# Kernel optimization log

Measured on AMD Instinct MI355X. Metric: run time of the kernel, lower is better.

Reference implementation:

```python
import jax, jax.numpy as jnp
import numpy as np
import math

HIDDEN = 1024
NUM_HEADS = 16
HEAD_DIM = 64
NUM_PREV = 4
BATCH = 4
SEQ = 1024
ROPE_BASE = 10000.0


def _rope(x):
    """Apply rotary embedding to x [..., seq, head_dim] (rotate-half form)."""
    d = x.shape[-1]
    s = x.shape[-2]
    inv_freq = 1.0 / (ROPE_BASE ** (jnp.arange(0, d, 2, dtype=jnp.float32) / d))
    ang = jnp.arange(s, dtype=jnp.float32)[:, None] * inv_freq[None, :]  # [s, d/2]
    cos, sin = jnp.cos(ang), jnp.sin(ang)
    x1, x2 = jnp.split(x, 2, axis=-1)
    return jnp.concatenate([x1 * cos - x2 * sin, x1 * sin + x2 * cos], axis=-1)


def setup_inputs() -> dict:
    key = jax.random.key(0)
    ks = jax.random.split(key, 8)
    std = 0.02
    d = {
        "hidden_states": jax.random.normal(ks[0], (BATCH, SEQ, HIDDEN), jnp.float32),
        "prev_hidden_states": jax.random.normal(ks[1], (NUM_PREV, BATCH, SEQ, HIDDEN), jnp.float32),
        "wq": jax.random.normal(ks[2], (HIDDEN, NUM_HEADS * HEAD_DIM), jnp.float32) * std,
        "bq": jnp.zeros((NUM_HEADS * HEAD_DIM,), jnp.float32),
        "wk": jax.random.normal(ks[3], (HIDDEN, NUM_HEADS * HEAD_DIM), jnp.float32) * std,
        "bk": jnp.zeros((NUM_HEADS * HEAD_DIM,), jnp.float32),
        "wv": jax.random.normal(ks[4], (HIDDEN, NUM_HEADS * HEAD_DIM), jnp.float32) * std,
        "bv": jnp.zeros((NUM_HEADS * HEAD_DIM,), jnp.float32),
        "wo": jax.random.normal(ks[5], (NUM_HEADS * HEAD_DIM, HIDDEN), jnp.float32) * std,
        "bo": jnp.zeros((HIDDEN,), jnp.float32),
        "wg": jax.random.normal(ks[6], (HIDDEN, NUM_PREV), jnp.float32) * std,
    }
    return d


def reference(hidden_states, prev_hidden_states, wq, bq, wk, bk, wv, bv, wo, bo, wg):
    B, S, H = hidden_states.shape
    P = prev_hidden_states.shape[0]
    nh, hd = NUM_HEADS, HEAD_DIM

    # Q projection + split heads + RoPE: [b, h, s, d]
    q = (hidden_states @ wq + bq).reshape(B, S, nh, hd).transpose(0, 2, 1, 3)
    q = _rope(q)

    # K/V projections for all prev layers at once: [p, b, h, s, d]
    k = (jnp.einsum('pbsh,he->pbse', prev_hidden_states, wk) + bk)
    k = k.reshape(P, B, S, nh, hd).transpose(0, 1, 3, 2, 4)
    k = _rope(k)
    v = (jnp.einsum('pbsh,he->pbse', prev_hidden_states, wv) + bv)
    v = v.reshape(P, B, S, nh, hd).transpose(0, 1, 3, 2, 4)

    # Attention per prev layer
    scale = 1.0 / math.sqrt(hd)
    attn = jnp.einsum('bhqd,pbhkd->pbhqk', q, k) * scale
    attn = jax.nn.softmax(attn, axis=-1)
    out = jnp.einsum('pbhqk,pbhkd->pbhqd', attn, v)  # [p, b, h, s, d]
    out = out.transpose(0, 1, 3, 2, 4).reshape(P, B, S, H)

    # Learned layer gating (faithful to original broadcast: requires B == P)
    pooled = jnp.mean(hidden_states, axis=1)            # [b, hidden]
    layer_w = jax.nn.softmax(pooled @ wg, axis=-1)      # [b, p]
    combined = jnp.sum(out * layer_w[:, :, None, None], axis=0)  # [b, s, hidden]

    return combined @ wo + bo
```

## Files before the change

### kernel.cpp

```cpp
#include <hip/hip_runtime.h>
#include <hip/hip_bf16.h>

#define B_  4
#define S_  1024
#define H_  1024
#define NH  16
#define HD  64
#define P_  4

typedef __attribute__((ext_vector_type(8))) short bf16x8;
typedef __attribute__((ext_vector_type(4))) float f32x4;
typedef __attribute__((ext_vector_type(16))) float f32x16;
typedef __attribute__((ext_vector_type(4))) unsigned int u32x4;

__device__ __forceinline__ float b2f(short s) {
  union { unsigned int u; float f; } v;
  v.u = ((unsigned int)(unsigned short)s) << 16;
  return v.f;
}
__device__ __forceinline__ short f2b(float f) {
  __hip_bfloat16 h = __float2bfloat16(f);
  return *reinterpret_cast<short*>(&h);
}
__device__ __forceinline__ float fast_exp2(float x) {
  float r;
  asm volatile("v_exp_f32 %0, %1" : "=v"(r) : "v"(x));
  return r;
}
__device__ __forceinline__ void gload_lds16(const void* g, void* l) {
  __builtin_amdgcn_global_load_lds(
      (const __attribute__((address_space(1))) unsigned int*)((uintptr_t)g),
      (__attribute__((address_space(3))) unsigned int*)((uintptr_t)l),
      16, 0, 0);
}

__global__ void prep_kernel(const float* __restrict__ hidden, const float* __restrict__ prev,
                            const float* __restrict__ wq, const float* __restrict__ wk,
                            const float* __restrict__ wv, const float* __restrict__ wo,
                            short* __restrict__ hbf, short* __restrict__ pbf,
                            short* __restrict__ wqT, short* __restrict__ wkT,
                            short* __restrict__ wvT, short* __restrict__ woT,
                            float* __restrict__ cost, float* __restrict__ sint,
                            float* __restrict__ pooled) {
  __shared__ short tile[32][33];
  int bid = blockIdx.x, tid = threadIdx.x;
  if (bid < 10240) {
    const float* src; short* dst; int idx;
    if (bid < 2048) { src = hidden; dst = hbf; idx = bid * 256 + tid; }
    else            { src = prev;   dst = pbf; idx = (bid - 2048) * 256 + tid; }
    const float4* s4 = (const float4*)(src + (size_t)idx * 8);
    float4 a = s4[0], b = s4[1];
    bf16x8 pk;
    pk[0] = f2b(a.x); pk[1] = f2b(a.y); pk[2] = f2b(a.z); pk[3] = f2b(a.w);
    pk[4] = f2b(b.x); pk[5] = f2b(b.y); pk[6] = f2b(b.z); pk[7] = f2b(b.w);
    *(bf16x8*)(dst + (size_t)idx * 8) = pk;
  } else if (bid < 14336) {
    int tb = bid - 10240;
    int z = tb >> 10, t = tb & 1023;
    const float* src = (z == 0) ? wq : (z == 1) ? wk : (z == 2) ? wv : wo;
    short*       dst = (z == 0) ? wqT : (z == 1) ? wkT : (z == 2) ? wvT : woT;
    int tx = tid & 31, ty = tid >> 5;
    int c0 = (t & 31) * 32, r0 = (t >> 5) * 32;
#pragma unroll
    for (int i = 0; i < 4; ++i)
      tile[ty + 8 * i][tx] = f2b(src[(r0 + ty + 8 * i) * 1024 + c0 + tx]);
    __syncthreads();
#pragma unroll
    for (int i = 0; i < 4; ++i)
      dst[(c0 + ty + 8 * i) * 1024 + r0 + tx] = tile[tx][ty + 8 * i];
  } else if (bid < 14464) {
    int idx = (bid - 14336) * 256 + tid;
    int s = idx >> 5, i = idx & 31;
    float invf = expf(-(float)i * (logf(10000.0f) / 32.0f));
    float a = (float)s * invf;
    cost[idx] = cosf(a);
    sint[idx] = sinf(a);
  } else {
    int idx = bid - 14464;
    int b = idx >> 5, chunk = idx & 31;
    const float* hp = hidden + (size_t)b * S_ * H_ + (size_t)chunk * 32 * H_ + tid * 4;
    float4 s = {0.f, 0.f, 0.f, 0.f};
#pragma unroll 4
    for (int t = 0; t < 32; ++t) {
      float4 v = *(const float4*)(hp + (size_t)t * H_);
      s.x += v.x; s.y += v.y; s.z += v.z; s.w += v.w;
    }
    float4 r;
    r.x = s.x * (1.0f / 1024.0f); r.y = s.y * (1.0f / 1024.0f);
    r.z = s.z * (1.0f / 1024.0f); r.w = s.w * (1.0f / 1024.0f);
    *(float4*)(pooled + (size_t)(b * 32 + chunk) * 1024 + tid * 4) = r;
  }
}

__global__ void gate_kernel(const float* __restrict__ pooled, const float* __restrict__ wg,
                            float* __restrict__ lw) {
  int w = threadIdx.x >> 6, lane = threadIdx.x & 63;
  float a0 = 0.f, a1 = 0.f, a2 = 0.f, a3 = 0.f;
  for (int e = lane; e < 1024; e += 64) {
    float pv = 0.f;
#pragma unroll
    for (int ch = 0; ch < 32; ++ch) pv += pooled[(size_t)(w * 32 + ch) * 1024 + e];
    a0 += pv * wg[e * 4 + 0];
    a1 += pv * wg[e * 4 + 1];
    a2 += pv * wg[e * 4 + 2];
    a3 += pv * wg[e * 4 + 3];
  }
#pragma unroll
  for (int off = 32; off > 0; off >>= 1) {
    a0 += __shfl_xor(a0, off, 64);
    a1 += __shfl_xor(a1, off, 64);
    a2 += __shfl_xor(a2, off, 64);
    a3 += __shfl_xor(a3, off, 64);
  }
  if (lane == 0) {
    float mx = fmaxf(fmaxf(a0, a1), fmaxf(a2, a3));
    float e0 = expf(a0 - mx), e1 = expf(a1 - mx), e2 = expf(a2 - mx), e3 = expf(a3 - mx);
    float inv = 1.0f / (e0 + e1 + e2 + e3);
    lw[w * 4 + 0] = e0 * inv;
    lw[w * 4 + 1] = e1 * inv;
    lw[w * 4 + 2] = e2 * inv;
    lw[w * 4 + 3] = e3 * inv;
  }
}

__device__ __forceinline__ void rope_epilogue(const f32x4 (&acc)[4][4], const float* __restrict__ bias,
                                              short* __restrict__ outp,
                                              const float* __restrict__ cost,
                                              const float* __restrict__ sint,
                                              int m0, int wm, int quad, int c, int hh) {
  float b0 = bias[hh * 64 + c];
  float b1 = bias[hh * 64 + 16 + c];
  float b2_ = bias[hh * 64 + 32 + c];
  float b3 = bias[hh * 64 + 48 + c];
#pragma unroll
  for (int mt = 0; mt < 4; ++mt) {
    int gm = m0 + wm * 64 + mt * 16 + quad * 4;
#pragma unroll
    for (int j = 0; j < 4; ++j) {
      int m = gm + j;
      int s = m & 1023;
      int bbx = m >> 10;
      int orow = ((bbx * NH + hh) * S_ + s) * HD;
      float c0f = cost[s * 32 + c], s0f = sint[s * 32 + c];
      float x1 = acc[mt][0][j] + b0, x2 = acc[mt][2][j] + b2_;
      outp[orow + c]      = f2b(x1 * c0f - x2 * s0f);
      outp[orow + 32 + c] = f2b(x1 * s0f + x2 * c0f);
      float c1f = cost[s * 32 + 16 + c], s1f = sint[s * 32 + 16 + c];
      float y1 = acc[mt][1][j] + b1, y2 = acc[mt][3][j] + b3;
      outp[orow + 16 + c] = f2b(y1 * c1f - y2 * s1f);
      outp[orow + 48 + c] = f2b(y1 * s1f + y2 * c1f);
    }
  }
}

__launch_bounds__(256, 2)
__global__ void qkv_gemm(const short* __restrict__ hbf, const short* __restrict__ pbf,
                         const short* __restrict__ BTq, const short* __restrict__ BTk,
                         const short* __restrict__ BTv,
                         const float* __restrict__ bq, const float* __restrict__ bk,
                         const float* __restrict__ bv,
                         short* __restrict__ outq, short* __restrict__ outk,
                         short* __restrict__ outv,
                         const float* __restrict__ cost, const float* __restrict__ sint) {
  __shared__ __align__(16) short As[128 * 64];
  __shared__ __align__(16) short Bs1[128 * 64];
  __shared__ __align__(16) short Bs2[128 * 64];
  int id = blockIdx.x;
  int xcd = id & 7;
  int local = id >> 3;
  int n0i = local & 7;
  int yl = local >> 3;
  int y = yl * 8 + xcd;
  int tid = threadIdx.x;
  int lane = tid & 63, wvv = tid >> 6;
  int quad = lane >> 4, c = lane & 15;
  int wm = wvv & 1, wn = wvv >> 1;
  bool isQ = y < 32;
  int m0 = (isQ ? y : (y - 32)) * 128;
  int n0 = n0i * 128;
  const short* A  = isQ ? hbf : pbf;
  const short* B1 = isQ ? BTq : BTk;
  f32x4 acc1[4][4] = {}, acc2[4][4] = {};
  const short* Ab = A + (size_t)m0 * 1024;
  const short* Bb1 = B1 + (size_t)n0 * 1024;
  const short* Bb2 = BTv + (size_t)n0 * 1024;
  int sr = tid >> 3, sch = tid & 7;

  for (int kb = 0; kb < 16; ++kb) {
    int k0 = kb * 64;
    __syncthreads();
#pragma unroll
    for (int rd = 0; rd < 4; ++rd) {
      int row = sr + rd * 32;
      int col = ((sch ^ (row & 7)) * 8) + k0;
      gload_lds16(Ab + row * 1024 + col,  As  + rd * 2048 + tid * 8);
      gload_lds16(Bb1 + row * 1024 + col, Bs1 + rd * 2048 + tid * 8);
      if (!isQ) gload_lds16(Bb2 + row * 1024 + col, Bs2 + rd * 2048 + tid * 8);
    }
    __syncthreads();
#pragma unroll
    for (int ko = 0; ko < 2; ++ko) {
      bf16x8 af[4], b1f[4];
#pragma unroll
      for (int mt = 0; mt < 4; ++mt) {
        int row = wm * 64 + mt * 16 + c;
        af[mt] = *(const bf16x8*)&As[row * 64 + (((ko * 4 + quad) ^ (row & 7)) * 8)];
      }
#pragma unroll
      for (int nt = 0; nt < 4; ++nt) {
        int row = wn * 64 + nt * 16 + c;
        b1f[nt] = *(const bf16x8*)&Bs1[row * 64 + (((ko * 4 + quad) ^ (row & 7)) * 8)];
      }
#pragma unroll
      for (int mt = 0; mt < 4; ++mt)
#pragma unroll
        for (int nt = 0; nt < 4; ++nt)
          acc1[mt][nt] = __builtin_amdgcn_mfma_f32_16x16x32_bf16(af[mt], b1f[nt], acc1[mt][nt], 0, 0, 0);
      if (!isQ) {
        bf16x8 b2f_[4];
#pragma unroll
        for (int nt = 0; nt < 4; ++nt) {
          int row = wn * 64 + nt * 16 + c;
          b2f_[nt] = *(const bf16x8*)&Bs2[row * 64 + (((ko * 4 + quad) ^ (row & 7)) * 8)];
        }
#pragma unroll
        for (int mt = 0; mt < 4; ++mt)
#pragma unroll
          for (int nt = 0; nt < 4; ++nt)
            acc2[mt][nt] = __builtin_amdgcn_mfma_f32_16x16x32_bf16(af[mt], b2f_[nt], acc2[mt][nt], 0, 0, 0);
      }
    }
  }

  int colb = n0 + wn * 64;
  int hh = colb >> 6;
  if (isQ) {
    rope_epilogue(acc1, bq, outq, cost, sint, m0, wm, quad, c, hh);
  } else {
    rope_epilogue(acc1, bk, outk, cost, sint, m0, wm, quad, c, hh);
    float bb[4];
#pragma unroll
    for (int nt = 0; nt < 4; ++nt) bb[nt] = bv[hh * 64 + nt * 16 + c];
#pragma unroll
    for (int mt = 0; mt < 4; ++mt) {
      int gm = m0 + wm * 64 + mt * 16 + quad * 4;
      int s4 = gm & 1023, pb = gm >> 10;
#pragma unroll
      for (int nt = 0; nt < 4; ++nt) {
        int d = nt * 16 + c;
        ushort4 pk;
        pk.x = (unsigned short)f2b(acc2[mt][nt][0] + bb[nt]);
        pk.y = (unsigned short)f2b(acc2[mt][nt][1] + bb[nt]);
        pk.z = (unsigned short)f2b(acc2[mt][nt][2] + bb[nt]);
        pk.w = (unsigned short)f2b(acc2[mt][nt][3] + bb[nt]);
        *(ushort4*)&outv[((pb * NH + hh) * HD + d) * S_ + s4] = pk;
      }
    }
  }
}

__launch_bounds__(256, 4)
__global__ void attn_kernel(const short* __restrict__ q, const short* __restrict__ k,
                            const short* __restrict__ vt, short* __restrict__ o) {
  int blk = blockIdx.x;
  int x = blk & 7, qt = (blk >> 3) & 7, g = blk >> 6;
  int pbh = g * 8 + x;
  int b = (pbh >> 4) & 3, h = pbh & 15;
  int tid = threadIdx.x;
  int w = tid >> 6, lane = tid & 63;
  int l31 = lane & 31, hh = lane >> 5;
  int r7 = l31 & 7;

  __shared__ __align__(16) short Klds[2][64 * 64];
  __shared__ __align__(16) short Vlds[2][64 * 64];
  __shared__ float lsumf[4][32];

  const short* qbase = q + ((size_t)(b * NH + h) * S_ + qt * 128 + w * 32 + l31) * HD + hh * 8;
  bf16x8 aq[4];
#pragma unroll
  for (int st4 = 0; st4 < 4; ++st4) aq[st4] = *(const bf16x8*)(qbase + st4 * 16);

  const short* kb = k + (size_t)pbh * S_ * HD;
  const short* vb = vt + (size_t)pbh * HD * S_;

  f32x16 O0 = {}, O1 = {};
  float ls0 = 0.f, ls1 = 0.f, ls2 = 0.f, ls3 = 0.f;
  const float cs = 0.18033688011f;

  int sr = tid >> 3;
  int lc = (tid & 7) ^ (sr & 7);

#define STAGE_KV(kt2, bufi) do {                                           \
    const short* ksrc = kb + ((kt2) * 64 + sr) * HD + lc * 8;              \
    gload_lds16(ksrc,           &Klds[bufi][tid * 8]);                     \
    gload_lds16(ksrc + 32 * HD, &Klds[bufi][2048 + tid * 8]);              \
    const short* vsrc = vb + (size_t)sr * S_ + (kt2) * 64 + lc * 8;        \
    gload_lds16(vsrc,           &Vlds[bufi][tid * 8]);                     \
    gload_lds16(vsrc + 32 * S_, &Vlds[bufi][2048 + tid * 8]);              \
  } while (0)

  STAGE_KV(0, 0);

  for (int kt = 0; kt < 16; ++kt) {
    int cb = kt & 1;
    if (kt < 15) {
      STAGE_KV(kt + 1, cb ^ 1);
      asm volatile("s_waitcnt vmcnt(4)" ::: "memory");
    } else {
      asm volatile("s_waitcnt vmcnt(0)" ::: "memory");
    }
    __builtin_amdgcn_s_barrier();
    __builtin_amdgcn_sched_barrier(0);

    u32x4 pa[4];
#pragma unroll
    for (int tau = 0; tau < 2; ++tau) {
      f32x16 st = {};
#pragma unroll
      for (int step = 0; step < 4; ++step) {
        bf16x8 kf = *(const bf16x8*)&Klds[cb][(tau * 32 + l31) * 64 + (((step * 2 + hh) ^ r7) * 8)];
        st = __builtin_amdgcn_mfma_f32_32x32x16_bf16(kf, aq[step], st, 0, 0, 0);
      }
      unsigned wb[8];
#pragma unroll
      for (int m = 0; m < 8; ++m) {
        float p0 = fast_exp2(st[2 * m] * cs);
        float p1 = fast_exp2(st[2 * m + 1] * cs);
        float ps = p0 + p1;
        if ((m & 3) == 0) ls0 += ps;
        else if ((m & 3) == 1) ls1 += ps;
        else if ((m & 3) == 2) ls2 += ps;
        else ls3 += ps;
        asm("v_cvt_pk_bf16_f32 %0, %1, %2" : "=v"(wb[m]) : "v"(p0), "v"(p1));
      }
#pragma unroll
      for (int gg = 0; gg < 2; ++gg) {
        unsigned x0 = wb[4 * gg + 0], y0 = wb[4 * gg + 2];
        unsigned x1 = wb[4 * gg + 1], y1 = wb[4 * gg + 3];
        asm volatile("v_permlane32_swap_b32 %0, %1" : "+v"(x0), "+v"(y0));
        asm volatile("v_permlane32_swap_b32 %0, %1" : "+v"(x1), "+v"(y1));
        u32x4 paw;
        paw[0] = x0; paw[1] = x1; paw[2] = y0; paw[3] = y1;
        pa[2 * tau + gg] = paw;
      }
    }

#pragma unroll
    for (int T = 0; T < 4; ++T) {
      bf16x8 ap = __builtin_bit_cast(bf16x8, pa[T]);
      bf16x8 vf0 = *(const bf16x8*)&Vlds[cb][l31 * 64 + (((T * 2 + hh) ^ r7) * 8)];
      O0 = __builtin_amdgcn_mfma_f32_32x32x16_bf16(ap, vf0, O0, 0, 0, 0);
      bf16x8 vf1 = *(const bf16x8*)&Vlds[cb][(32 + l31) * 64 + (((T * 2 + hh) ^ r7) * 8)];
      O1 = __builtin_amdgcn_mfma_f32_32x32x16_bf16(ap, vf1, O1, 0, 0, 0);
    }

    __builtin_amdgcn_s_barrier();
  }
#undef STAGE_KV

  float lsum = (ls0 + ls1) + (ls2 + ls3);
  lsum += __shfl_xor(lsum, 32, 64);
  if (lane < 32) lsumf[w][l31] = lsum;

  short* ob = o + ((size_t)pbh * S_ + qt * 128 + w * 32) * HD;
#pragma unroll
  for (int gg = 0; gg < 4; ++gg) {
    f32x4 lv = *(const f32x4*)&lsumf[w][4 * hh + 8 * gg];
#pragma unroll
    for (int j = 0; j < 4; ++j) {
      float inv = 1.0f / lv[j];
      int qrow = 4 * hh + 8 * gg + j;
      ob[qrow * HD + l31]      = f2b(O0[4 * gg + j] * inv);
      ob[qrow * HD + 32 + l31] = f2b(O1[4 * gg + j] * inv);
    }
  }
}

__global__ void combine_kernel(const short* __restrict__ o, const float* __restrict__ lw,
                               short* __restrict__ comb) {
  int idx = blockIdx.x * 256 + threadIdx.x;
  int e8 = idx & 127;
  int s = (idx >> 7) & 1023;
  int b = idx >> 17;
  int h = e8 >> 3, d0 = (e8 & 7) * 8;
  float acc[8] = {};
#pragma unroll
  for (int p = 0; p < 4; ++p) {
    float wgt = lw[p * 4 + b];
    const short* op = o + (((size_t)(p * 4 + b) * NH + h) * S_ + s) * HD + d0;
    bf16x8 v = *(const bf16x8*)op;
#pragma unroll
    for (int i = 0; i < 8; ++i) acc[i] += wgt * b2f(v[i]);
  }
  bf16x8 pk;
#pragma unroll
  for (int i = 0; i < 8; ++i) pk[i] = f2b(acc[i]);
  *(bf16x8*)&comb[((size_t)b * S_ + s) * H_ + e8 * 8] = pk;
}

__launch_bounds__(256, 4)
__global__ void gemm_out(const short* __restrict__ A, const short* __restrict__ BT,
                         const float* __restrict__ bias, float* __restrict__ outf) {
  __shared__ __align__(16) short As[64 * 64];
  __shared__ __align__(16) short Bs[128 * 64];
  int id = blockIdx.x;
  int xcd = id & 7;
  int local = id >> 3;
  int n0i = local & 7;
  int yl = local >> 3;
  int y = yl * 8 + xcd;
  int tid = threadIdx.x;
  int lane = tid & 63, wvv = tid >> 6;
  int quad = lane >> 4, c = lane & 15;
  int wm = wvv & 1, wn = wvv >> 1;
  int m0 = y * 64, n0 = n0i * 128;
  f32x4 acc[2][4] = {};
  const short* Ab = A + (size_t)m0 * 1024;
  const short* Bb = BT + (size_t)n0 * 1024;
  int sr = tid >> 3, sch = tid & 7;

  for (int kb = 0; kb < 16; ++kb) {
    int k0 = kb * 64;
    __syncthreads();
#pragma unroll
    for (int rd = 0; rd < 2; ++rd) {
      int row = sr + rd * 32;
      int col = ((sch ^ (row & 7)) * 8) + k0;
      gload_lds16(Ab + row * 1024 + col, As + rd * 2048 + tid * 8);
    }
#pragma unroll
    for (int rd = 0; rd < 4; ++rd) {
      int row = sr + rd * 32;
      int col = ((sch ^ (row & 7)) * 8) + k0;
      gload_lds16(Bb + row * 1024 + col, Bs + rd * 2048 + tid * 8);
    }
    __syncthreads();
#pragma unroll
    for (int ko = 0; ko < 2; ++ko) {
      bf16x8 af[2], bfr[4];
#pragma unroll
      for (int mt = 0; mt < 2; ++mt) {
        int row = wm * 32 + mt * 16 + c;
        af[mt] = *(const bf16x8*)&As[row * 64 + (((ko * 4 + quad) ^ (row & 7)) * 8)];
      }
#pragma unroll
      for (int nt = 0; nt < 4; ++nt) {
        int row = wn * 64 + nt * 16 + c;
        bfr[nt] = *(const bf16x8*)&Bs[row * 64 + (((ko * 4 + quad) ^ (row & 7)) * 8)];
      }
#pragma unroll
      for (int mt = 0; mt < 2; ++mt)
#pragma unroll
        for (int nt = 0; nt < 4; ++nt)
          acc[mt][nt] = __builtin_amdgcn_mfma_f32_16x16x32_bf16(af[mt], bfr[nt], acc[mt][nt], 0, 0, 0);
    }
  }

  int colb = n0 + wn * 64;
  float bb[4];
#pragma unroll
  for (int nt = 0; nt < 4; ++nt) bb[nt] = bias[colb + nt * 16 + c];
#pragma unroll
  for (int mt = 0; mt < 2; ++mt) {
    int gm = m0 + wm * 32 + mt * 16 + quad * 4;
#pragma unroll
    for (int j = 0; j < 4; ++j) {
      int m = gm + j;
#pragma unroll
      for (int nt = 0; nt < 4; ++nt)
        outf[(size_t)m * 1024 + colb + nt * 16 + c] = acc[mt][nt][j] + bb[nt];
    }
  }
}

extern "C" void kernel_launch(void* const* d_in, const int* in_sizes, int n_in,
                              void* d_out, int out_size, void* d_ws, size_t ws_size,
                              hipStream_t stream) {
  (void)in_sizes; (void)n_in; (void)out_size; (void)ws_size;
  const float* hidden = (const float*)d_in[0];
  const float* prev   = (const float*)d_in[1];
  const float* wq = (const float*)d_in[2];
  const float* bq = (const float*)d_in[3];
  const float* wk = (const float*)d_in[4];
  const float* bk = (const float*)d_in[5];
  const float* wv = (const float*)d_in[6];
  const float* bv = (const float*)d_in[7];
  const float* wo = (const float*)d_in[8];
  const float* bo = (const float*)d_in[9];
  const float* wg = (const float*)d_in[10];
  float* out = (float*)d_out;
  char* ws = (char*)d_ws;

  size_t off = 0;
  short* wqT = (short*)(ws + off); off += (size_t)1024 * 1024 * 2;
  short* wkT = (short*)(ws + off); off += (size_t)1024 * 1024 * 2;
  short* wvT = (short*)(ws + off); off += (size_t)1024 * 1024 * 2;
  short* woT = (short*)(ws + off); off += (size_t)1024 * 1024 * 2;
  short* hbf = (short*)(ws + off); off += (size_t)B_ * S_ * H_ * 2;
  short* pbf = (short*)(ws + off); off += (size_t)P_ * B_ * S_ * H_ * 2;
  short* qbf = (short*)(ws + off); off += (size_t)B_ * S_ * H_ * 2;
  short* kbf = (short*)(ws + off); off += (size_t)P_ * B_ * S_ * H_ * 2;
  short* vtb = (short*)(ws + off); off += (size_t)P_ * B_ * S_ * H_ * 2;
  float* cost = (float*)(ws + off); off += (size_t)S_ * 32 * 4;
  float* sint = (float*)(ws + off); off += (size_t)S_ * 32 * 4;
  float* pooled = (float*)(ws + off); off += (size_t)B_ * 32 * 1024 * 4;
  float* lw = (float*)(ws + off); off += 64;
  short* obf  = pbf;
  short* comb = qbf;

  prep_kernel<<<14592, 256, 0, stream>>>(hidden, prev, wq, wk, wv, wo,
                                         hbf, pbf, wqT, wkT, wvT, woT,
                                         cost, sint, pooled);
  gate_kernel<<<1, 256, 0, stream>>>(pooled, wg, lw);
  qkv_gemm<<<1280, 256, 0, stream>>>(hbf, pbf, wqT, wkT, wvT,
                                     bq, bk, bv, qbf, kbf, vtb, cost, sint);
  attn_kernel<<<2048, 256, 0, stream>>>(qbf, kbf, vtb, obf);
  combine_kernel<<<2048, 256, 0, stream>>>(obf, lw, comb);
  gemm_out<<<512, 256, 0, stream>>>(comb, woT, bo, out);
}
```

Before: 348.0 us.

## Double-buffer QKV GEMM LDS tiles to overlap global loads with MFMA

Restructures the QKV projection GEMM main loop to use two half-depth LDS buffers (K-step 32 instead of 64) and prefetches the next K slice with async global-to-LDS loads while computing the current one. Explicit vmcnt waits and raw barriers replace the double __syncthreads per iteration. The new layout packs two rows per 64-element LDS line with a matching XOR swizzle. The cost is twice as many loop iterations and barriers, and correctness now depends on hand-counted vmcnt values.

Measured after the change: 355.7 us. +2.2%, slower.

```diff
diff --git a/kernel.cpp b/kernel.cpp
--- a/kernel.cpp
+++ b/kernel.cpp
@@ -162,9 +162,9 @@
                          short* __restrict__ outq, short* __restrict__ outk,
                          short* __restrict__ outv,
                          const float* __restrict__ cost, const float* __restrict__ sint) {
-  __shared__ __align__(16) short As[128 * 64];
-  __shared__ __align__(16) short Bs1[128 * 64];
-  __shared__ __align__(16) short Bs2[128 * 64];
+  __shared__ __align__(16) short As[2][64 * 64];
+  __shared__ __align__(16) short Bs1[2][64 * 64];
+  __shared__ __align__(16) short Bs2[2][64 * 64];
   int id = blockIdx.x;
   int xcd = id & 7;
   int local = id >> 3;
@@ -184,53 +184,72 @@
   const short* Ab = A + (size_t)m0 * 1024;
   const short* Bb1 = B1 + (size_t)n0 * 1024;
   const short* Bb2 = BTv + (size_t)n0 * 1024;
-  int sr = tid >> 3, sch = tid & 7;
-
-  for (int kb = 0; kb < 16; ++kb) {
-    int k0 = kb * 64;
-    __syncthreads();
-#pragma unroll
-    for (int rd = 0; rd < 4; ++rd) {
-      int row = sr + rd * 32;
-      int col = ((sch ^ (row & 7)) * 8) + k0;
-      gload_lds16(Ab + row * 1024 + col,  As  + rd * 2048 + tid * 8);
-      gload_lds16(Bb1 + row * 1024 + col, Bs1 + rd * 2048 + tid * 8);
-      if (!isQ) gload_lds16(Bb2 + row * 1024 + col, Bs2 + rd * 2048 + tid * 8);
-    }
-    __syncthreads();
-#pragma unroll
-    for (int ko = 0; ko < 2; ++ko) {
-      bf16x8 af[4], b1f[4];
-#pragma unroll
-      for (int mt = 0; mt < 4; ++mt) {
-        int row = wm * 64 + mt * 16 + c;
-        af[mt] = *(const bf16x8*)&As[row * 64 + (((ko * 4 + quad) ^ (row & 7)) * 8)];
-      }
+
+  int lr0 = tid >> 3, ch0 = tid & 7;
+  int lr1 = lr0 + 32;
+  int lc0 = ch0 ^ (lr0 & 7), lc1 = ch0 ^ (lr1 & 7);
+  int am0 = 2 * lr0 + (lc0 >> 2), ak0 = (lc0 & 3) * 8;
+  int am1 = 2 * lr1 + (lc1 >> 2), ak1 = (lc1 & 3) * 8;
+
+#define STAGEQKV(bufi, k0s) do {                                             \
+    gload_lds16(Ab  + (size_t)am0 * 1024 + (k0s) + ak0, &As[bufi][tid * 8]); \
+    gload_lds16(Ab  + (size_t)am1 * 1024 + (k0s) + ak1, &As[bufi][(256 + tid) * 8]); \
+    gload_lds16(Bb1 + (size_t)am0 * 1024 + (k0s) + ak0, &Bs1[bufi][tid * 8]); \
+    gload_lds16(Bb1 + (size_t)am1 * 1024 + (k0s) + ak1, &Bs1[bufi][(256 + tid) * 8]); \
+    if (!isQ) {                                                              \
+      gload_lds16(Bb2 + (size_t)am0 * 1024 + (k0s) + ak0, &Bs2[bufi][tid * 8]); \
+      gload_lds16(Bb2 + (size_t)am1 * 1024 + (k0s) + ak1, &Bs2[bufi][(256 + tid) * 8]); \
+    }                                                                        \
+  } while (0)
+#define FRAG_OFF(r, q) (((r) >> 1) * 64 + (((((r) & 1) * 4 + (q)) ^ (((r) >> 1) & 7)) * 8))
+
+  STAGEQKV(0, 0);
+
+  for (int kb = 0; kb < 32; ++kb) {
+    int cb = kb & 1;
+    if (kb < 31) {
+      STAGEQKV(cb ^ 1, (kb + 1) * 32);
+      if (isQ) asm volatile("s_waitcnt vmcnt(4)" ::: "memory");
+      else     asm volatile("s_waitcnt vmcnt(6)" ::: "memory");
+    } else {
+      asm volatile("s_waitcnt vmcnt(0)" ::: "memory");
+    }
+    __builtin_amdgcn_s_barrier();
+    __builtin_amdgcn_sched_barrier(0);
+
+    bf16x8 af[4], b1f[4];
+#pragma unroll
+    for (int mt = 0; mt < 4; ++mt) {
+      int r = wm * 64 + mt * 16 + c;
+      af[mt] = *(const bf16x8*)&As[cb][FRAG_OFF(r, quad)];
+    }
+#pragma unroll
+    for (int nt = 0; nt < 4; ++nt) {
+      int r = wn * 64 + nt * 16 + c;
+      b1f[nt] = *(const bf16x8*)&Bs1[cb][FRAG_OFF(r, quad)];
+    }
+#pragma unroll
+    for (int mt = 0; mt < 4; ++mt)
+#pragma unroll
+      for (int nt = 0; nt < 4; ++nt)
+        acc1[mt][nt] = __builtin_amdgcn_mfma_f32_16x16x32_bf16(af[mt], b1f[nt], acc1[mt][nt], 0, 0, 0);
+    if (!isQ) {
+      bf16x8 b2f_[4];
 #pragma unroll
       for (int nt = 0; nt < 4; ++nt) {
-        int row = wn * 64 + nt * 16 + c;
-        b1f[nt] = *(const bf16x8*)&Bs1[row * 64 + (((ko * 4 + quad) ^ (row & 7)) * 8)];
+        int r = wn * 64 + nt * 16 + c;
+        b2f_[nt] = *(const bf16x8*)&Bs2[cb][FRAG_OFF(r, quad)];
       }
 #pragma unroll
       for (int mt = 0; mt < 4; ++mt)
 #pragma unroll
         for (int nt = 0; nt < 4; ++nt)
-          acc1[mt][nt] = __builtin_amdgcn_mfma_f32_16x16x32_bf16(af[mt], b1f[nt], acc1[mt][nt], 0, 0, 0);
-      if (!isQ) {
-        bf16x8 b2f_[4];
-#pragma unroll
-        for (int nt = 0; nt < 4; ++nt) {
-          int row = wn * 64 + nt * 16 + c;
-          b2f_[nt] = *(const bf16x8*)&Bs2[row * 64 + (((ko * 4 + quad) ^ (row & 7)) * 8)];
-        }
-#pragma unroll
-        for (int mt = 0; mt < 4; ++mt)
-#pragma unroll
-          for (int nt = 0; nt < 4; ++nt)
-            acc2[mt][nt] = __builtin_amdgcn_mfma_f32_16x16x32_bf16(af[mt], b2f_[nt], acc2[mt][nt], 0, 0, 0);
-      }
-    }
-  }
+          acc2[mt][nt] = __builtin_amdgcn_mfma_f32_16x16x32_bf16(af[mt], b2f_[nt], acc2[mt][nt], 0, 0, 0);
+    }
+    __builtin_amdgcn_s_barrier();
+  }
+#undef STAGEQKV
+#undef FRAG_OFF
 
   int colb = n0 + wn * 64;
   int hh = colb >> 6;
```

## Fuse layer-gated combine into attention kernel looping over prev layers

Applied to the files above, without the earlier changes.

Each attention block now loops over the four previous layers for its (batch, head, q-tile). It scales each layer's normalized output by the gate weight and accumulates it in registers, then writes the combined bf16 result straight into the layout the output GEMM reads. This removes the separate combine kernel and the round trip of per-layer attention outputs through global memory. The trade-off is a 4x smaller grid (512 blocks) with a lower occupancy hint, which may reduce latency hiding. The gate kernel is also split across four blocks with vectorized loads.

Result: faster. 332.7 us (-4.4%).

```diff
diff --git a/kernel.cpp b/kernel.cpp
--- a/kernel.cpp
+++ b/kernel.cpp
@@ -94,32 +94,41 @@
 
 __global__ void gate_kernel(const float* __restrict__ pooled, const float* __restrict__ wg,
                             float* __restrict__ lw) {
-  int w = threadIdx.x >> 6, lane = threadIdx.x & 63;
-  float a0 = 0.f, a1 = 0.f, a2 = 0.f, a3 = 0.f;
-  for (int e = lane; e < 1024; e += 64) {
-    float pv = 0.f;
-#pragma unroll
-    for (int ch = 0; ch < 32; ++ch) pv += pooled[(size_t)(w * 32 + ch) * 1024 + e];
-    a0 += pv * wg[e * 4 + 0];
-    a1 += pv * wg[e * 4 + 1];
-    a2 += pv * wg[e * 4 + 2];
-    a3 += pv * wg[e * 4 + 3];
-  }
-#pragma unroll
-  for (int off = 32; off > 0; off >>= 1) {
-    a0 += __shfl_xor(a0, off, 64);
-    a1 += __shfl_xor(a1, off, 64);
-    a2 += __shfl_xor(a2, off, 64);
-    a3 += __shfl_xor(a3, off, 64);
-  }
+  __shared__ float red[4][4];
+  int b = blockIdx.x, tid = threadIdx.x;
+  int w = tid >> 6, lane = tid & 63;
+  int e0 = tid * 4;
+  float4 pv = {0.f, 0.f, 0.f, 0.f};
+#pragma unroll 4
+  for (int ch = 0; ch < 32; ++ch) {
+    float4 v = *(const float4*)&pooled[(size_t)(b * 32 + ch) * 1024 + e0];
+    pv.x += v.x; pv.y += v.y; pv.z += v.z; pv.w += v.w;
+  }
+  float a[4];
+#pragma unroll
+  for (int j = 0; j < 4; ++j)
+    a[j] = pv.x * wg[(e0 + 0) * 4 + j] + pv.y * wg[(e0 + 1) * 4 + j] +
+           pv.z * wg[(e0 + 2) * 4 + j] + pv.w * wg[(e0 + 3) * 4 + j];
+#pragma unroll
+  for (int off = 32; off > 0; off >>= 1)
+#pragma unroll
+    for (int j = 0; j < 4; ++j) a[j] += __shfl_xor(a[j], off, 64);
   if (lane == 0) {
-    float mx = fmaxf(fmaxf(a0, a1), fmaxf(a2, a3));
-    float e0 = expf(a0 - mx), e1 = expf(a1 - mx), e2 = expf(a2 - mx), e3 = expf(a3 - mx);
-    float inv = 1.0f / (e0 + e1 + e2 + e3);
-    lw[w * 4 + 0] = e0 * inv;
-    lw[w * 4 + 1] = e1 * inv;
-    lw[w * 4 + 2] = e2 * inv;
-    lw[w * 4 + 3] = e3 * inv;
+    red[w][0] = a[0]; red[w][1] = a[1]; red[w][2] = a[2]; red[w][3] = a[3];
+  }
+  __syncthreads();
+  if (tid == 0) {
+    float s0 = red[0][0] + red[1][0] + red[2][0] + red[3][0];
+    float s1 = red[0][1] + red[1][1] + red[2][1] + red[3][1];
+    float s2 = red[0][2] + red[1][2] + red[2][2] + red[3][2];
+    float s3 = red[0][3] + red[1][3] + red[2][3] + red[3][3];
+    float mx = fmaxf(fmaxf(s0, s1), fmaxf(s2, s3));
+    float e0_ = expf(s0 - mx), e1 = expf(s1 - mx), e2 = expf(s2 - mx), e3 = expf(s3 - mx);
+    float inv = 1.0f / (e0_ + e1 + e2 + e3);
+    lw[b * 4 + 0] = e0_ * inv;
+    lw[b * 4 + 1] = e1 * inv;
+    lw[b * 4 + 2] = e2 * inv;
+    lw[b * 4 + 3] = e3 * inv;
   }
 }
 
@@ -259,13 +268,14 @@
   }
 }
 
-__launch_bounds__(256, 4)
+__launch_bounds__(256, 2)
 __global__ void attn_kernel(const short* __restrict__ q, const short* __restrict__ k,
-                            const short* __restrict__ vt, short* __restrict__ o) {
+                            const short* __restrict__ vt, const float* __restrict__ lw,
+                            short* __restrict__ comb) {
   int blk = blockIdx.x;
   int x = blk & 7, qt = (blk >> 3) & 7, g = blk >> 6;
-  int pbh = g * 8 + x;
-  int b = (pbh >> 4) & 3, h = pbh & 15;
+  int bh = g * 8 + x;
+  int b = bh >> 4, h = bh & 15;
   int tid = threadIdx.x;
   int w = tid >> 6, lane = tid & 63;
   int l31 = lane & 31, hh = lane >> 5;
@@ -280,122 +290,123 @@
 #pragma unroll
   for (int st4 = 0; st4 < 4; ++st4) aq[st4] = *(const bf16x8*)(qbase + st4 * 16);
 
-  const short* kb = k + (size_t)pbh * S_ * HD;
-  const short* vb = vt + (size_t)pbh * HD * S_;
-
-  f32x16 O0 = {}, O1 = {};
-  float ls0 = 0.f, ls1 = 0.f, ls2 = 0.f, ls3 = 0.f;
+  float wl0 = lw[b], wl1 = lw[4 + b], wl2 = lw[8 + b], wl3 = lw[12 + b];
+
+  const short* kbase = k + (size_t)(b * 16 + h) * S_ * HD;
+  const short* vbase = vt + (size_t)(b * 16 + h) * HD * S_;
+  const size_t pstr = (size_t)64 * S_ * HD;
+
+  f32x16 C0 = {}, C1 = {};
   const float cs = 0.18033688011f;
 
   int sr = tid >> 3;
   int lc = (tid & 7) ^ (sr & 7);
 
-#define STAGE_KV(kt2, bufi) do {                                           \
-    const short* ksrc = kb + ((kt2) * 64 + sr) * HD + lc * 8;              \
+#define STAGE_KV(kb2, vb2, kt2, bufi) do {                                 \
+    const short* ksrc = (kb2) + ((kt2) * 64 + sr) * HD + lc * 8;           \
     gload_lds16(ksrc,           &Klds[bufi][tid * 8]);                     \
     gload_lds16(ksrc + 32 * HD, &Klds[bufi][2048 + tid * 8]);              \
-    const short* vsrc = vb + (size_t)sr * S_ + (kt2) * 64 + lc * 8;        \
+    const short* vsrc = (vb2) + (size_t)sr * S_ + (kt2) * 64 + lc * 8;     \
     gload_lds16(vsrc,           &Vlds[bufi][tid * 8]);                     \
     gload_lds16(vsrc + 32 * S_, &Vlds[bufi][2048 + tid * 8]);              \
   } while (0)
 
-  STAGE_KV(0, 0);
-
-  for (int kt = 0; kt < 16; ++kt) {
-    int cb = kt & 1;
-    if (kt < 15) {
-      STAGE_KV(kt + 1, cb ^ 1);
-      asm volatile("s_waitcnt vmcnt(4)" ::: "memory");
-    } else {
-      asm volatile("s_waitcnt vmcnt(0)" ::: "memory");
-    }
-    __builtin_amdgcn_s_barrier();
-    __builtin_amdgcn_sched_barrier(0);
-
-    u32x4 pa[4];
-#pragma unroll
-    for (int tau = 0; tau < 2; ++tau) {
-      f32x16 st = {};
-#pragma unroll
-      for (int step = 0; step < 4; ++step) {
-        bf16x8 kf = *(const bf16x8*)&Klds[cb][(tau * 32 + l31) * 64 + (((step * 2 + hh) ^ r7) * 8)];
-        st = __builtin_amdgcn_mfma_f32_32x32x16_bf16(kf, aq[step], st, 0, 0, 0);
-      }
-      unsigned wb[8];
-#pragma unroll
-      for (int m = 0; m < 8; ++m) {
-        float p0 = fast_exp2(st[2 * m] * cs);
-        float p1 = fast_exp2(st[2 * m + 1] * cs);
-        float ps = p0 + p1;
-        if ((m & 3) == 0) ls0 += ps;
-        else if ((m & 3) == 1) ls1 += ps;
-        else if ((m & 3) == 2) ls2 += ps;
-        else ls3 += ps;
-        asm("v_cvt_pk_bf16_f32 %0, %1, %2" : "=v"(wb[m]) : "v"(p0), "v"(p1));
-      }
-#pragma unroll
-      for (int gg = 0; gg < 2; ++gg) {
-        unsigned x0 = wb[4 * gg + 0], y0 = wb[4 * gg + 2];
-        unsigned x1 = wb[4 * gg + 1], y1 = wb[4 * gg + 3];
-        asm volatile("v_permlane32_swap_b32 %0, %1" : "+v"(x0), "+v"(y0));
-        asm volatile("v_permlane32_swap_b32 %0, %1" : "+v"(x1), "+v"(y1));
-        u32x4 paw;
-        paw[0] = x0; paw[1] = x1; paw[2] = y0; paw[3] = y1;
-        pa[2 * tau + gg] = paw;
-      }
-    }
-
-#pragma unroll
-    for (int T = 0; T < 4; ++T) {
-      bf16x8 ap = __builtin_bit_cast(bf16x8, pa[T]);
-      bf16x8 vf0 = *(const bf16x8*)&Vlds[cb][l31 * 64 + (((T * 2 + hh) ^ r7) * 8)];
-      O0 = __builtin_amdgcn_mfma_f32_32x32x16_bf16(ap, vf0, O0, 0, 0, 0);
-      bf16x8 vf1 = *(const bf16x8*)&Vlds[cb][(32 + l31) * 64 + (((T * 2 + hh) ^ r7) * 8)];
-      O1 = __builtin_amdgcn_mfma_f32_32x32x16_bf16(ap, vf1, O1, 0, 0, 0);
-    }
-
-    __builtin_amdgcn_s_barrier();
+  STAGE_KV(kbase, vbase, 0, 0);
+
+#pragma unroll 1
+  for (int p = 0; p < 4; ++p) {
+    f32x16 O0 = {}, O1 = {};
+    float ls0 = 0.f, ls1 = 0.f, ls2 = 0.f, ls3 = 0.f;
+
+#pragma unroll 1
+    for (int kt = 0; kt < 16; ++kt) {
+      int t = p * 16 + kt;
+      int cb = t & 1;
+      if (t < 63) {
+        int t1 = t + 1;
+        int p2 = t1 >> 4, kt2 = t1 & 15;
+        const short* kb2 = kbase + (size_t)p2 * pstr;
+        const short* vb2 = vbase + (size_t)p2 * pstr;
+        STAGE_KV(kb2, vb2, kt2, cb ^ 1);
+        asm volatile("s_waitcnt vmcnt(4)" ::: "memory");
+      } else {
+        asm volatile("s_waitcnt vmcnt(0)" ::: "memory");
+      }
+      __builtin_amdgcn_s_barrier();
+      __builtin_amdgcn_sched_barrier(0);
+
+      u32x4 pa[4];
+#pragma unroll
+      for (int tau = 0; tau < 2; ++tau) {
+        f32x16 st = {};
+#pragma unroll
+        for (int step = 0; step < 4; ++step) {
+          bf16x8 kf = *(const bf16x8*)&Klds[cb][(tau * 32 + l31) * 64 + (((step * 2 + hh) ^ r7) * 8)];
+          st = __builtin_amdgcn_mfma_f32_32x32x16_bf16(kf, aq[step], st, 0, 0, 0);
+        }
+        unsigned wb[8];
+#pragma unroll
+        for (int m = 0; m < 8; ++m) {
+          float p0 = fast_exp2(st[2 * m] * cs);
+          float p1 = fast_exp2(st[2 * m + 1] * cs);
+          float ps = p0 + p1;
+          if ((m & 3) == 0) ls0 += ps;
+          else if ((m & 3) == 1) ls1 += ps;
+          else if ((m & 3) == 2) ls2 += ps;
+          else ls3 += ps;
+          asm("v_cvt_pk_bf16_f32 %0, %1, %2" : "=v"(wb[m]) : "v"(p0), "v"(p1));
+        }
+#pragma unroll
+        for (int gg = 0; gg < 2; ++gg) {
+          unsigned x0 = wb[4 * gg + 0], y0 = wb[4 * gg + 2];
+          unsigned x1 = wb[4 * gg + 1], y1 = wb[4 * gg + 3];
+          asm volatile("v_permlane32_swap_b32 %0, %1" : "+v"(x0), "+v"(y0));
+          asm volatile("v_permlane32_swap_b32 %0, %1" : "+v"(x1), "+v"(y1));
+          u32x4 paw;
+          paw[0] = x0; paw[1] = x1; paw[2] = y0; paw[3] = y1;
+          pa[2 * tau + gg] = paw;
+        }
+      }
+
+#pragma unroll
+      for (int T = 0; T < 4; ++T) {
+        bf16x8 ap = __builtin_bit_cast(bf16x8, pa[T]);
+        bf16x8 vf0 = *(const bf16x8*)&Vlds[cb][l31 * 64 + (((T * 2 + hh) ^ r7) * 8)];
+        O0 = __builtin_amdgcn_mfma_f32_32x32x16_bf16(ap, vf0, O0, 0, 0, 0);
+        bf16x8 vf1 = *(const bf16x8*)&Vlds[cb][(32 + l31) * 64 + (((T * 2 + hh) ^ r7) * 8)];
+        O1 = __builtin_amdgcn_mfma_f32_32x32x16_bf16(ap, vf1, O1, 0, 0, 0);
+      }
+
+      __builtin_amdgcn_s_barrier();
+    }
+
+    float lsum = (ls0 + ls1) + (ls2 + ls3);
+    lsum += __shfl_xor(lsum, 32, 64);
+    if (lane < 32) lsumf[w][l31] = lsum;
+    float wl = (p == 0) ? wl0 : (p == 1) ? wl1 : (p == 2) ? wl2 : wl3;
+#pragma unroll
+    for (int gg = 0; gg < 4; ++gg) {
+      f32x4 lv = *(const f32x4*)&lsumf[w][4 * hh + 8 * gg];
+#pragma unroll
+      for (int j = 0; j < 4; ++j) {
+        float sc = wl / lv[j];
+        C0[4 * gg + j] += O0[4 * gg + j] * sc;
+        C1[4 * gg + j] += O1[4 * gg + j] * sc;
+      }
+    }
   }
 #undef STAGE_KV
 
-  float lsum = (ls0 + ls1) + (ls2 + ls3);
-  lsum += __shfl_xor(lsum, 32, 64);
-  if (lane < 32) lsumf[w][l31] = lsum;
-
-  short* ob = o + ((size_t)pbh * S_ + qt * 128 + w * 32) * HD;
+  short* ob = comb + ((size_t)b * S_ + qt * 128 + w * 32) * H_ + h * 64;
 #pragma unroll
   for (int gg = 0; gg < 4; ++gg) {
-    f32x4 lv = *(const f32x4*)&lsumf[w][4 * hh + 8 * gg];
 #pragma unroll
     for (int j = 0; j < 4; ++j) {
-      float inv = 1.0f / lv[j];
       int qrow = 4 * hh + 8 * gg + j;
-      ob[qrow * HD + l31]      = f2b(O0[4 * gg + j] * inv);
-      ob[qrow * HD + 32 + l31] = f2b(O1[4 * gg + j] * inv);
-    }
-  }
-}
-
-__global__ void combine_kernel(const short* __restrict__ o, const float* __restrict__ lw,
-                               short* __restrict__ comb) {
-  int idx = blockIdx.x * 256 + threadIdx.x;
-  int e8 = idx & 127;
-  int s = (idx >> 7) & 1023;
-  int b = idx >> 17;
-  int h = e8 >> 3, d0 = (e8 & 7) * 8;
-  float acc[8] = {};
-#pragma unroll
-  for (int p = 0; p < 4; ++p) {
-    float wgt = lw[p * 4 + b];
-    const short* op = o + (((size_t)(p * 4 + b) * NH + h) * S_ + s) * HD + d0;
-    bf16x8 v = *(const bf16x8*)op;
-#pragma unroll
-    for (int i = 0; i < 8; ++i) acc[i] += wgt * b2f(v[i]);
-  }
-  bf16x8 pk;
-#pragma unroll
-  for (int i = 0; i < 8; ++i) pk[i] = f2b(acc[i]);
-  *(bf16x8*)&comb[((size_t)b * S_ + s) * H_ + e8 * 8] = pk;
+      ob[(size_t)qrow * H_ + l31]      = f2b(C0[4 * gg + j]);
+      ob[(size_t)qrow * H_ + 32 + l31] = f2b(C1[4 * gg + j]);
+    }
+  }
 }
 
 __launch_bounds__(256, 4)
@@ -505,16 +516,14 @@
   float* sint = (float*)(ws + off); off += (size_t)S_ * 32 * 4;
   float* pooled = (float*)(ws + off); off += (size_t)B_ * 32 * 1024 * 4;
   float* lw = (float*)(ws + off); off += 64;
-  short* obf  = pbf;
-  short* comb = qbf;
+  short* comb = pbf;
 
   prep_kernel<<<14592, 256, 0, stream>>>(hidden, prev, wq, wk, wv, wo,
                                          hbf, pbf, wqT, wkT, wvT, woT,
                                          cost, sint, pooled);
-  gate_kernel<<<1, 256, 0, stream>>>(pooled, wg, lw);
+  gate_kernel<<<4, 256, 0, stream>>>(pooled, wg, lw);
   qkv_gemm<<<1280, 256, 0, stream>>>(hbf, pbf, wqT, wkT, wvT,
                                      bq, bk, bv, qbf, kbf, vtb, cost, sint);
-  attn_kernel<<<2048, 256, 0, stream>>>(qbf, kbf, vtb, obf);
-  combine_kernel<<<2048, 256, 0, stream>>>(obf, lw, comb);
+  attn_kernel<<<512, 256, 0, stream>>>(qbf, kbf, vtb, lw, comb);
   gemm_out<<<512, 256, 0, stream>>>(comb, woT, bo, out);
 }
```
